# Optimization experiments

Hardware: AMD Instinct MI355X
Metric: run time of the kernel (lower is better)

The kernel has to match this reference:

```python
import jax, jax.numpy as jnp
import numpy as np

_LEVELS = jnp.array([-4, -2, -1, 0, 1, 2, 4], dtype=jnp.int32)  # shift-quant 7-value grid 'A'

B, S = 1, 512
IN_F, OUT_F = 4096, 16384
BLOCK = 64
NUM_BLOCKS = (IN_F + BLOCK - 1) // BLOCK  # 64


def setup_inputs() -> dict:
    key = jax.random.key(0)
    k1, k2, k3, k4 = jax.random.split(key, 4)
    x = jax.random.normal(k1, (B, S, IN_F), dtype=jnp.float32)
    idx = jax.random.randint(k2, (OUT_F, IN_F), 0, 7)
    q_weight = _LEVELS[idx]  # int32 values in {-4,-2,-1,0,1,2,4}
    scales = (jax.random.uniform(k3, (OUT_F, NUM_BLOCKS), dtype=jnp.float32) * 0.05 + 0.001).astype(jnp.float16)
    bias = (jax.random.normal(k4, (OUT_F,), dtype=jnp.float32) * 0.02).astype(jnp.float16)
    return {"x": x, "q_weight": q_weight, "scales": scales, "bias": bias, "block_size": BLOCK}


def reference(x, q_weight, scales, bias, block_size):
    # shift_matmul: dequantize blockwise-scaled power-of-two int8 weights, then GEMM.
    out_f, in_f = q_weight.shape
    # broadcast per-block fp16 scales along the in_features axis (handles padding block)
    w_scale = jnp.repeat(scales.astype(jnp.float32), block_size, axis=1)[:, :in_f]  # [out, in]
    w = q_weight.astype(jnp.float32) * w_scale  # [out, in]
    out = jnp.einsum("bsi,oi->bso", x, w)
    out = out + bias.astype(out.dtype)
    return out.astype(x.dtype)
```

## Files before the change

### kernel.cpp

```cpp
#include <hip/hip_runtime.h>
#include <hip/hip_bf16.h>
#include <stdint.h>


#define MM 512
#define NN 16384
#define KK 4096
#define BN 64
#define BK 128
#define NKB (KK / BK)
#define NSLAB (NN / BN)

typedef __bf16 bf16x8 __attribute__((ext_vector_type(8)));
typedef float floatx4 __attribute__((ext_vector_type(4)));

__device__ __forceinline__ unsigned int pk_bf16_rtn(float lo, float hi) {
    __hip_bfloat162 h = __float22bfloat162_rn(float2{lo, hi});
    return *reinterpret_cast<unsigned int*>(&h);
}

__device__ __forceinline__ uint4 deq8(const int4 q0, const int4 q1, const float s) {
    uint4 u;
    u.x = pk_bf16_rtn((float)q0.x * s, (float)q0.y * s);
    u.y = pk_bf16_rtn((float)q0.z * s, (float)q0.w * s);
    u.z = pk_bf16_rtn((float)q1.x * s, (float)q1.y * s);
    u.w = pk_bf16_rtn((float)q1.z * s, (float)q1.w * s);
    return u;
}

__device__ __forceinline__ void gload16(const void* g, void* l) {
    __builtin_amdgcn_global_load_lds(
        (const __attribute__((address_space(1))) void*)g,
        (__attribute__((address_space(3))) void*)l, 16, 0, 0);
}

__global__ __launch_bounds__(256) void pack_x(const float* __restrict__ x,
                                              unsigned short* __restrict__ xp) {
    const int t    = blockIdx.x * 256 + threadIdx.x;
    const int lane = t & 63;
    const int mt   = (t >> 6) & 31;
    const int ks   = (t >> 11) & 3;
    const int kb   = t >> 13;
    const int m    = mt * 16 + (lane & 15);
    const int k    = kb * 128 + ks * 32 + (lane >> 4) * 8;
    const float* px = x + (size_t)m * KK + k;
    const float4 a = *(const float4*)px;
    const float4 b = *(const float4*)(px + 4);
    uint4 o;
    o.x = pk_bf16_rtn(a.x, a.y);
    o.y = pk_bf16_rtn(a.z, a.w);
    o.z = pk_bf16_rtn(b.x, b.y);
    o.w = pk_bf16_rtn(b.z, b.w);
    *(uint4*)(xp + (size_t)t * 8) = o;
}

__global__ __launch_bounds__(256) void pack_w(const int* __restrict__ qw,
                                              const float* __restrict__ scales,
                                              unsigned short* __restrict__ wb) {
    __shared__ unsigned short lw[64][136];
    const int tile = blockIdx.x;
    const int slab = tile >> 5;
    const int kb   = tile & 31;
    const int u    = threadIdx.x;

    const int r   = u >> 2;
    const int q   = u & 3;
    const int col = slab * 64 + r;
    const int k0  = kb * 128 + q * 32;
    const int* qp = qw + (size_t)col * KK + k0;
    const float s = scales[(size_t)col * 64 + (k0 >> 6)];
#pragma unroll
    for (int i = 0; i < 4; ++i) {
        const int4 q0 = *(const int4*)(qp + i * 8);
        const int4 q1 = *(const int4*)(qp + i * 8 + 4);
        const uint4 uu = deq8(q0, q1, s);
        *(uint4*)&lw[r][q * 32 + i * 8] = uu;
    }
    __syncthreads();

    unsigned short* wt = wb + (size_t)tile * 8192;
#pragma unroll
    for (int hc = 0; hc < 4; ++hc) {
        const int c  = u + hc * 256;
        const int f  = c >> 6;
        const int l  = c & 63;
        const int ks = f >> 2;
        const int j  = f & 3;
        const uint4 v = *(const uint4*)&lw[j * 16 + (l & 15)][ks * 32 + (l >> 4) * 8];
        *(uint4*)(wt + (size_t)c * 8) = v;
    }
}

__global__ __launch_bounds__(512, 4) void qlin_gemm(
    const unsigned short* __restrict__ xp,
    const unsigned short* __restrict__ wb,
    const float* __restrict__ bias,
    float* __restrict__ out)
{
    __shared__ unsigned short sB[2][BN * BK];

    const int t    = threadIdx.x;
    const int lane = t & 63;
    const int wv   = t >> 6;
    const int ln   = lane & 15;
    const int quad = lane >> 4;
    const int slab = blockIdx.x & 255;
    const int h    = blockIdx.x >> 8;
    const int n0   = slab * BN;

    const unsigned short* wbase = wb + (size_t)slab * 32 * 8192;

    floatx4 acc[2][4];
#pragma unroll
    for (int i = 0; i < 2; ++i)
#pragma unroll
        for (int j = 0; j < 4; ++j)
            acc[i][j] = (floatx4)0.0f;

    {
        const unsigned short* src = wbase + (size_t)t * 8;
        gload16(src,            &sB[0][wv * 512]);
        gload16(src + 512 * 8,  &sB[0][4096 + wv * 512]);
    }
    __syncthreads();

    for (int kb = 0; kb < NKB; ++kb) {
        const unsigned short* sb = sB[kb & 1];

        if (kb + 1 < NKB) {
            const unsigned short* src = wbase + (size_t)(kb + 1) * 8192 + (size_t)t * 8;
            unsigned short* d0 = &sB[(kb + 1) & 1][wv * 512];
            unsigned short* d1 = &sB[(kb + 1) & 1][4096 + wv * 512];
            gload16(src,           d0);
            gload16(src + 512 * 8, d1);
        }

        bf16x8 a[4][2];
#pragma unroll
        for (int ks = 0; ks < 4; ++ks) {
            const unsigned short* ap =
                xp + (size_t)kb * 65536
                   + (size_t)((ks * 32 + h * 16 + wv * 2) * 64 + lane) * 8;
            a[ks][0] = *(const bf16x8*)(ap);
            a[ks][1] = *(const bf16x8*)(ap + 512);
        }

#pragma unroll
        for (int ks = 0; ks < 4; ++ks) {
#pragma unroll
            for (int jj = 0; jj < 4; jj += 2) {
                bf16x8 b0 = *(const bf16x8*)(sb + ((ks * 4 + jj) * 64 + lane) * 8);
                bf16x8 b1 = *(const bf16x8*)(sb + ((ks * 4 + jj + 1) * 64 + lane) * 8);
                acc[0][jj]     = __builtin_amdgcn_mfma_f32_16x16x32_bf16(a[ks][0], b0, acc[0][jj], 0, 0, 0);
                acc[1][jj]     = __builtin_amdgcn_mfma_f32_16x16x32_bf16(a[ks][1], b0, acc[1][jj], 0, 0, 0);
                acc[0][jj + 1] = __builtin_amdgcn_mfma_f32_16x16x32_bf16(a[ks][0], b1, acc[0][jj + 1], 0, 0, 0);
                acc[1][jj + 1] = __builtin_amdgcn_mfma_f32_16x16x32_bf16(a[ks][1], b1, acc[1][jj + 1], 0, 0, 0);
            }
        }

        if (kb + 1 < NKB) __syncthreads();
    }

#pragma unroll
    for (int j = 0; j < 4; ++j) {
        const int n = n0 + j * 16 + ln;
        const float bv = bias[n];
#pragma unroll
        for (int i = 0; i < 2; ++i) {
            const int mbase = h * 256 + wv * 32 + i * 16 + quad * 4;
#pragma unroll
            for (int rr = 0; rr < 4; ++rr)
                out[(size_t)(mbase + rr) * NN + n] = acc[i][j][rr] + bv;
        }
    }
}

__global__ __launch_bounds__(256) void qlin_naive(
    const float* __restrict__ x, const int* __restrict__ qw,
    const float* __restrict__ scales, const float* __restrict__ bias,
    float* __restrict__ out) {
    const int n = blockIdx.x * 256 + threadIdx.x;
    const int m = blockIdx.y;
    if (n >= NN || m >= MM) return;
    float accv = 0.0f;
    for (int kb = 0; kb < 64; ++kb) {
        const float s = scales[(size_t)n * 64 + kb];
        float part = 0.0f;
        for (int k = kb * 64; k < kb * 64 + 64; ++k)
            part += x[(size_t)m * KK + k] * (float)qw[(size_t)n * KK + k];
        accv += part * s;
    }
    out[(size_t)m * NN + n] = accv + bias[n];
}

extern "C" void kernel_launch(void* const* d_in, const int* in_sizes, int n_in,
                              void* d_out, int out_size, void* d_ws, size_t ws_size,
                              hipStream_t stream) {
    const float* x    = (const float*)d_in[0];
    const int* qw     = (const int*)d_in[1];
    const float* scl  = (const float*)d_in[2];
    const float* bias = (const float*)d_in[3];
    float* out        = (float*)d_out;

    const size_t XPB = (size_t)MM * KK * sizeof(unsigned short);
    const size_t WBB = (size_t)NN * KK * sizeof(unsigned short);

    if (ws_size >= XPB + WBB) {
        unsigned short* xp = (unsigned short*)d_ws;
        unsigned short* wb = (unsigned short*)((char*)d_ws + XPB);
        pack_x<<<dim3(MM * KK / (256 * 8)), dim3(256), 0, stream>>>(x, xp);
        pack_w<<<dim3(NSLAB * 32), dim3(256), 0, stream>>>(qw, scl, wb);
        qlin_gemm<<<dim3(NSLAB * 2), dim3(512), 0, stream>>>(xp, wb, bias, out);
    } else {
        qlin_naive<<<dim3(NN / 256, MM), dim3(256), 0, stream>>>(x, qw, scl, bias, out);
    }
}
```

Before: 490.1 us.

## Coalesce weight dequant loads and double-buffer A fragments in GEMM

pack_w now reads q_weight with consecutive threads covering contiguous 16-byte chunks of each row and stages the per-block scales in shared memory, replacing the old pattern of 128-byte strided per-thread reads. The GEMM loop is unrolled by two with ping-pong register sets for the A fragments, so the next k-block's global A loads are issued before the current block's MFMAs run. This hides A-load latency behind compute at the cost of more vector registers, which may pressure occupancy under the 512x4 launch bound.

```diff
diff --git a/kernel.cpp b/kernel.cpp
--- a/kernel.cpp
+++ b/kernel.cpp
@@ -17,15 +17,6 @@
 __device__ __forceinline__ unsigned int pk_bf16_rtn(float lo, float hi) {
     __hip_bfloat162 h = __float22bfloat162_rn(float2{lo, hi});
     return *reinterpret_cast<unsigned int*>(&h);
-}
-
-__device__ __forceinline__ uint4 deq8(const int4 q0, const int4 q1, const float s) {
-    uint4 u;
-    u.x = pk_bf16_rtn((float)q0.x * s, (float)q0.y * s);
-    u.y = pk_bf16_rtn((float)q0.z * s, (float)q0.w * s);
-    u.z = pk_bf16_rtn((float)q1.x * s, (float)q1.y * s);
-    u.w = pk_bf16_rtn((float)q1.z * s, (float)q1.w * s);
-    return u;
 }
 
 __device__ __forceinline__ void gload16(const void* g, void* l) {
@@ -57,31 +48,36 @@
 __global__ __launch_bounds__(256) void pack_w(const int* __restrict__ qw,
                                               const float* __restrict__ scales,
                                               unsigned short* __restrict__ wb) {
-    __shared__ unsigned short lw[64][136];
+    __shared__ unsigned short lw[64][132];
+    __shared__ float ls[128];
     const int tile = blockIdx.x;
     const int slab = tile >> 5;
     const int kb   = tile & 31;
     const int u    = threadIdx.x;
 
-    const int r   = u >> 2;
-    const int q   = u & 3;
-    const int col = slab * 64 + r;
-    const int k0  = kb * 128 + q * 32;
-    const int* qp = qw + (size_t)col * KK + k0;
-    const float s = scales[(size_t)col * 64 + (k0 >> 6)];
-#pragma unroll
-    for (int i = 0; i < 4; ++i) {
-        const int4 q0 = *(const int4*)(qp + i * 8);
-        const int4 q1 = *(const int4*)(qp + i * 8 + 4);
-        const uint4 uu = deq8(q0, q1, s);
-        *(uint4*)&lw[r][q * 32 + i * 8] = uu;
-    }
+    if (u < 128)
+        ls[u] = scales[(size_t)(slab * 64 + (u >> 1)) * 64 + kb * 2 + (u & 1)];
     __syncthreads();
 
+    const int* qbase = qw + (size_t)slab * 64 * KK + kb * 128;
+#pragma unroll
+    for (int i = 0; i < 8; ++i) {
+        const int c  = i * 256 + u;
+        const int r  = c >> 5;
+        const int kk = (c & 31) * 4;
+        const int4 q = *(const int4*)(qbase + (size_t)r * KK + kk);
+        const float s = ls[r * 2 + ((c & 31) >> 4)];
+        uint2 o;
+        o.x = pk_bf16_rtn((float)q.x * s, (float)q.y * s);
+        o.y = pk_bf16_rtn((float)q.z * s, (float)q.w * s);
+        *(uint2*)&lw[r][kk] = o;
+    }
+    __syncthreads();
+
     unsigned short* wt = wb + (size_t)tile * 8192;
 #pragma unroll
     for (int hc = 0; hc < 4; ++hc) {
-        const int c  = u + hc * 256;
+        const int c  = hc * 256 + u;
         const int f  = c >> 6;
         const int l  = c & 63;
         const int ks = f >> 2;
@@ -90,6 +86,42 @@
         *(uint4*)(wt + (size_t)c * 8) = v;
     }
 }
+
+#define STAGE_B(KB, BUF)                                                        \
+    {                                                                           \
+        const unsigned short* src_ = wbase + (size_t)(KB) * 8192 + (size_t)t * 8; \
+        gload16(src_,           &sB[BUF][wv * 512]);                            \
+        gload16(src_ + 512 * 8, &sB[BUF][4096 + wv * 512]);                     \
+    }
+
+#define LOAD_A(DST, KB)                                                         \
+    {                                                                           \
+        const unsigned short* ap_ =                                             \
+            xp + (size_t)(KB) * 65536                                           \
+               + (size_t)((h * 16 + wv * 2) * 64 + lane) * 8;                   \
+        _Pragma("unroll")                                                       \
+        for (int ks = 0; ks < 4; ++ks) {                                        \
+            DST[ks][0] = *(const bf16x8*)(ap_ + ks * 16384);                    \
+            DST[ks][1] = *(const bf16x8*)(ap_ + ks * 16384 + 512);              \
+        }                                                                       \
+    }
+
+#define COMPUTE(BUF, A)                                                         \
+    {                                                                           \
+        const unsigned short* sb_ = sB[BUF];                                    \
+        _Pragma("unroll")                                                       \
+        for (int ks = 0; ks < 4; ++ks) {                                        \
+            _Pragma("unroll")                                                   \
+            for (int jj = 0; jj < 4; jj += 2) {                                 \
+                bf16x8 b0 = *(const bf16x8*)(sb_ + ((ks * 4 + jj) * 64 + lane) * 8);     \
+                bf16x8 b1 = *(const bf16x8*)(sb_ + ((ks * 4 + jj + 1) * 64 + lane) * 8); \
+                acc[0][jj]     = __builtin_amdgcn_mfma_f32_16x16x32_bf16(A[ks][0], b0, acc[0][jj], 0, 0, 0);     \
+                acc[1][jj]     = __builtin_amdgcn_mfma_f32_16x16x32_bf16(A[ks][1], b0, acc[1][jj], 0, 0, 0);     \
+                acc[0][jj + 1] = __builtin_amdgcn_mfma_f32_16x16x32_bf16(A[ks][0], b1, acc[0][jj + 1], 0, 0, 0); \
+                acc[1][jj + 1] = __builtin_amdgcn_mfma_f32_16x16x32_bf16(A[ks][1], b1, acc[1][jj + 1], 0, 0, 0); \
+            }                                                                   \
+        }                                                                       \
+    }
 
 __global__ __launch_bounds__(512, 4) void qlin_gemm(
     const unsigned short* __restrict__ xp,
@@ -117,48 +149,24 @@
         for (int j = 0; j < 4; ++j)
             acc[i][j] = (floatx4)0.0f;
 
-    {
-        const unsigned short* src = wbase + (size_t)t * 8;
-        gload16(src,            &sB[0][wv * 512]);
-        gload16(src + 512 * 8,  &sB[0][4096 + wv * 512]);
-    }
+    bf16x8 aA[4][2], aB[4][2];
+
+    STAGE_B(0, 0)
+    LOAD_A(aA, 0)
     __syncthreads();
 
-    for (int kb = 0; kb < NKB; ++kb) {
-        const unsigned short* sb = sB[kb & 1];
-
-        if (kb + 1 < NKB) {
-            const unsigned short* src = wbase + (size_t)(kb + 1) * 8192 + (size_t)t * 8;
-            unsigned short* d0 = &sB[(kb + 1) & 1][wv * 512];
-            unsigned short* d1 = &sB[(kb + 1) & 1][4096 + wv * 512];
-            gload16(src,           d0);
-            gload16(src + 512 * 8, d1);
+    for (int kb = 0; kb < NKB; kb += 2) {
+        STAGE_B(kb + 1, 1)
+        LOAD_A(aB, kb + 1)
+        COMPUTE(0, aA)
+        __syncthreads();
+
+        if (kb + 2 < NKB) {
+            STAGE_B(kb + 2, 0)
+            LOAD_A(aA, kb + 2)
         }
-
-        bf16x8 a[4][2];
-#pragma unroll
-        for (int ks = 0; ks < 4; ++ks) {
-            const unsigned short* ap =
-                xp + (size_t)kb * 65536
-                   + (size_t)((ks * 32 + h * 16 + wv * 2) * 64 + lane) * 8;
-            a[ks][0] = *(const bf16x8*)(ap);
-            a[ks][1] = *(const bf16x8*)(ap + 512);
-        }
-
-#pragma unroll
-        for (int ks = 0; ks < 4; ++ks) {
-#pragma unroll
-            for (int jj = 0; jj < 4; jj += 2) {
-                bf16x8 b0 = *(const bf16x8*)(sb + ((ks * 4 + jj) * 64 + lane) * 8);
-                bf16x8 b1 = *(const bf16x8*)(sb + ((ks * 4 + jj + 1) * 64 + lane) * 8);
-                acc[0][jj]     = __builtin_amdgcn_mfma_f32_16x16x32_bf16(a[ks][0], b0, acc[0][jj], 0, 0, 0);
-                acc[1][jj]     = __builtin_amdgcn_mfma_f32_16x16x32_bf16(a[ks][1], b0, acc[1][jj], 0, 0, 0);
-                acc[0][jj + 1] = __builtin_amdgcn_mfma_f32_16x16x32_bf16(a[ks][0], b1, acc[0][jj + 1], 0, 0, 0);
-                acc[1][jj + 1] = __builtin_amdgcn_mfma_f32_16x16x32_bf16(a[ks][1], b1, acc[1][jj + 1], 0, 0, 0);
-            }
-        }
-
-        if (kb + 1 < NKB) __syncthreads();
+        COMPUTE(1, aB)
+        if (kb + 2 < NKB) __syncthreads();
     }
 
 #pragma unroll
```

Measured after the change: 493.2 us. About the same (+0.6%).
